# Kernel tuning notes

Hardware: AMD Instinct MI355X
Metric: run time of the kernel (lower is better)

The kernel has to match this reference:

```python
import jax, jax.numpy as jnp
import numpy as np

B, N, D = 8, 4096, 256
K = 8192

def setup_inputs() -> dict:
    key = jax.random.key(0)
    k1, k2 = jax.random.split(key)
    x = jax.random.normal(k1, (B, N, D), dtype=jnp.float32)
    codebook = jax.random.normal(k2, (K, D), dtype=jnp.float32)
    return {"x": x, "codebook": codebook}

def reference(x, codebook):
    """Euclidean VQ forward: cdist + argmin nearest-codebook assignment,
    straight-through quantization, commitment loss, and the scatter-based
    EMA statistics (cluster counts and per-cluster sums)."""
    b, n, d = x.shape
    k = codebook.shape[0]
    flat = x.reshape(-1, d)                                  # [BN, D]
    x2 = jnp.sum(flat * flat, axis=-1, keepdims=True)        # [BN, 1]
    c2 = jnp.sum(codebook * codebook, axis=-1)               # [K]
    dist = x2 + c2[None, :] - 2.0 * (flat @ codebook.T)      # [BN, K]
    embed_ind = jnp.argmin(dist, axis=-1)                    # [BN]
    quantize = codebook[embed_ind].reshape(b, n, d)          # gather
    # commitment loss (codebook detached, as in EMA codebooks)
    commit_loss = jnp.mean((jax.lax.stop_gradient(quantize) - x) ** 2)
    # straight-through estimator
    quantize_st = x + jax.lax.stop_gradient(quantize - x)
    # EMA codebook-update statistics (scatter / segment reductions)
    cluster_size = jax.ops.segment_sum(
        jnp.ones_like(embed_ind, dtype=x.dtype), embed_ind, num_segments=k)  # [K]
    embed_sum = jax.ops.segment_sum(flat, embed_ind, num_segments=k)         # [K, D]
    return quantize_st, embed_ind.reshape(b, n), commit_loss, cluster_size, embed_sum
```

## Files before the change

kernel.cpp:

```cpp
#include <hip/hip_runtime.h>
#include <hip/hip_bf16.h>
#include <math.h>

#define DIM 256
#define KCODES 8192
#define BN_TOTAL 32768

#define OUT_IND 8388608
#define OUT_LOSS 8421376
#define OUT_CS 8421377
#define OUT_ES 8429569
#define OUT_TOTAL 10526721

#define XI8_OFF 0
#define CI8_OFF 4194304
#define PART_OFF OUT_ES

typedef unsigned short u16;
typedef unsigned char u8;
typedef unsigned int u32;
typedef __attribute__((ext_vector_type(4))) int i32x4;
typedef __attribute__((address_space(1))) const void gvoid_t;
typedef __attribute__((address_space(3))) void lvoid_t;

#define QSCALE (127.0f / 6.0f)
#define INV_2S2 (16129.0f / 72.0f)

__global__ __launch_bounds__(256) void vq_prep(const float* __restrict__ x,
                                               const float* __restrict__ cb,
                                               u8* __restrict__ Xi8,
                                               u8* __restrict__ Ci8,
                                               float* __restrict__ c2,
                                               int* __restrict__ c2i) {
  int b = blockIdx.x;
  bool isx = (b < 2048);
  int g = (isx ? b : (b - 2048)) * 256 + threadIdx.x;
  int row = g >> 4;
  int chunk = g & 15;
  const float* src = (isx ? x : cb) + (size_t)row * DIM + chunk * 16;
  float vv[16];
#pragma unroll
  for (int q = 0; q < 4; ++q) {
    float4 v = *(const float4*)(src + q * 4);
    vv[q * 4 + 0] = v.x; vv[q * 4 + 1] = v.y;
    vv[q * 4 + 2] = v.z; vv[q * 4 + 3] = v.w;
  }
  u32 w[4];
  float s = 0.0f;
#pragma unroll
  for (int q = 0; q < 4; ++q) {
    u32 acc = 0;
#pragma unroll
    for (int e = 0; e < 4; ++e) {
      float v = vv[q * 4 + e];
      s += v * v;
      float vs = fminf(fmaxf(v * QSCALE, -127.0f), 127.0f);
      int iv = (int)rintf(vs);
      acc |= ((u32)(u8)(char)iv) << (8 * e);
    }
    w[q] = acc;
  }
  uint4 pk = {w[0], w[1], w[2], w[3]};
  if (isx) {
    *(uint4*)(Xi8 + (size_t)row * DIM + chunk * 16) = pk;
  } else {
    int kbg = chunk >> 2;
    int j = chunk & 3;
    int js = j ^ ((row >> 1) & 3);
    *(uint4*)(Ci8 + (size_t)row * DIM + kbg * 64 + js * 16) = pk;
#pragma unroll
    for (int m = 1; m <= 8; m <<= 1) s += __shfl_xor(s, m, 64);
    if (chunk == 0) {
      c2[row] = s;
      c2i[row] = (int)rintf((s - 256.0f) * INV_2S2);
    }
  }
}

__global__ __launch_bounds__(256, 4)
void vq_mfma(const u8* __restrict__ XB, const u8* __restrict__ CBb,
             const int* __restrict__ c2i, int2* __restrict__ partials) {
  __shared__ __align__(16) u8 As[2][128][64];
  const int t = threadIdx.x;
  const int wid = t >> 6;
  const int lane = t & 63;
  const int lhi = lane >> 4, llo = lane & 15;
  const int sl = lhi ^ ((llo >> 1) & 3);
  const int wm = wid & 1;
  const int wn = wid >> 1;
  const int rt = blockIdx.x & 511;
  const int s = blockIdx.x >> 9;
  const int row0 = rt * 64;
  const int code0base = s * 4096;

  i32x4 b[2][4];
#pragma unroll
  for (int n = 0; n < 2; ++n) {
    const u8* bp = XB + (size_t)(row0 + wn * 32 + n * 16 + llo) * DIM + lhi * 16;
#pragma unroll
    for (int kb = 0; kb < 4; ++kb)
      b[n][kb] = *(const i32x4*)(bp + kb * 64);
  }

  char* AsB = (char*)As;
  const int srow = lane >> 2;
  const int scol = (lane & 3) << 4;

  const int p0 = wid * 2, p1 = wid * 2 + 1;
  const u8* lb0 = CBb + (size_t)(code0base + p0 * 16 + srow) * DIM + scol;
  const u8* lb1 = CBb + (size_t)(code0base + p1 * 16 + srow) * DIM + scol;
  char* dp0 = AsB + (p0 << 10);
  char* dp1 = AsB + (p1 << 10);

  auto STAGE = [&](u32 srcoff, int d) {
    __builtin_amdgcn_global_load_lds((gvoid_t*)(lb0 + srcoff),
                                     (lvoid_t*)(dp0 + (d << 13)), 16, 0, 0);
    __builtin_amdgcn_global_load_lds((gvoid_t*)(lb1 + srcoff),
                                     (lvoid_t*)(dp1 + (d << 13)), 16, 0, 0);
  };

  int v1[2], v2[2];
#pragma unroll
  for (int n = 0; n < 2; ++n) { v1[n] = 0x7FFFFFFF; v2[n] = 0x7FFFFFFF; }

  STAGE(0, 0);
  u32 ctoff = 0;

#pragma unroll 1
  for (int ct = 0; ct < 32; ++ct) {
    const int code0 = code0base + ct * 128;
    i32x4 acc[4][2];
#pragma unroll
    for (int m = 0; m < 4; ++m)
#pragma unroll
      for (int n = 0; n < 2; ++n) acc[m][n] = (i32x4){0, 0, 0, 0};

#pragma unroll
    for (int kb = 0; kb < 4; ++kb) {
      const int cc = ct * 4 + kb;
      __syncthreads();
      if (cc < 127) {
        u32 noff = (kb == 3) ? (ctoff + 32768u) : (ctoff + (u32)(kb + 1) * 64u);
        STAGE(noff, (cc + 1) & 1);
      }
      const char* src = AsB + ((cc & 1) << 13);
      i32x4 a[4];
#pragma unroll
      for (int m = 0; m < 4; ++m)
        a[m] = *(const i32x4*)(src + ((wm * 64 + m * 16 + llo) << 6) + (sl << 4));
#pragma unroll
      for (int m = 0; m < 4; ++m)
#pragma unroll
        for (int n = 0; n < 2; ++n)
          acc[m][n] = __builtin_amdgcn_mfma_i32_16x16x64_i8(a[m], b[n][kb],
                                                            acc[m][n], 0, 0, 0);
      if (kb == 3) {
#pragma unroll
        for (int m = 0; m < 4; ++m) {
          int cbase = code0 + wm * 64 + m * 16 + lhi * 4;
          int4 cv = *(const int4*)(c2i + cbase);
          int cvv[4] = {cv.x, cv.y, cv.z, cv.w};
#pragma unroll
          for (int n = 0; n < 2; ++n) {
#pragma unroll
            for (int r = 0; r < 4; ++r) {
              int diff = cvv[r] - acc[m][n][r];
              int key = (int)(((u32)diff << 13) + (u32)(cbase + r));
              int ov1 = v1[n];
              v1[n] = min(key, ov1);
              v2[n] = min(v2[n], max(key, ov1));
            }
          }
        }
      }
    }
    ctoff += 32768u;
  }
#pragma unroll
  for (int n = 0; n < 2; ++n) {
    int row = row0 + wn * 32 + n * 16 + llo;
    int slot = s * 8 + wm * 4 + lhi;
    partials[(size_t)row * 16 + slot] = make_int2(v1[n], v2[n]);
  }
}

__global__ __launch_bounds__(256)
void vq_pick(const float* __restrict__ x, const float* __restrict__ cb,
             const float* __restrict__ c2g, const int2* __restrict__ partials,
             int* __restrict__ ind, float* __restrict__ out_ind,
             float* __restrict__ out_q, int* __restrict__ cnt,
             float* __restrict__ loss_part) {
  __shared__ float lsm[4];
  int wid = threadIdx.x >> 6, lane = threadIdx.x & 63;
  int row = blockIdx.x * 4 + wid;
  int cv = 0x7FFFFFFF, cv2 = 0x7FFFFFFF;
  if (lane < 16) {
    int2 p = partials[(size_t)row * 16 + lane];
    cv = p.x; cv2 = p.y;
  }
  int cand[4];
#pragma unroll
  for (int rsel = 0; rsel < 4; ++rsel) {
    int bv = cv;
#pragma unroll
    for (int mask = 1; mask < 16; mask <<= 1)
      bv = min(bv, __shfl_xor(bv, mask, 64));
    bv = __shfl(bv, 0, 64);
    cand[rsel] = bv & 8191;
    if (cv == bv) { cv = cv2; cv2 = 0x7FFFFFFF; }
  }
  const float4 xv = *(const float4*)(x + (size_t)row * DIM + lane * 4);
  float4 q0 = *(const float4*)(cb + (size_t)cand[0] * DIM + lane * 4);
  float4 q1 = *(const float4*)(cb + (size_t)cand[1] * DIM + lane * 4);
  float4 q2 = *(const float4*)(cb + (size_t)cand[2] * DIM + lane * 4);
  float4 q3 = *(const float4*)(cb + (size_t)cand[3] * DIM + lane * 4);
  float d0 = xv.x * q0.x + xv.y * q0.y + xv.z * q0.z + xv.w * q0.w;
  float d1 = xv.x * q1.x + xv.y * q1.y + xv.z * q1.z + xv.w * q1.w;
  float d2 = xv.x * q2.x + xv.y * q2.y + xv.z * q2.z + xv.w * q2.w;
  float d3 = xv.x * q3.x + xv.y * q3.y + xv.z * q3.z + xv.w * q3.w;
  float x2 = xv.x * xv.x + xv.y * xv.y + xv.z * xv.z + xv.w * xv.w;
#pragma unroll
  for (int mask = 1; mask < 64; mask <<= 1) {
    d0 += __shfl_xor(d0, mask, 64);
    d1 += __shfl_xor(d1, mask, 64);
    d2 += __shfl_xor(d2, mask, 64);
    d3 += __shfl_xor(d3, mask, 64);
    x2 += __shfl_xor(x2, mask, 64);
  }
  float e0 = fmaf(-2.0f, d0, c2g[cand[0]]);
  float e1 = fmaf(-2.0f, d1, c2g[cand[1]]);
  float e2 = fmaf(-2.0f, d2, c2g[cand[2]]);
  float e3 = fmaf(-2.0f, d3, c2g[cand[3]]);
  float best = e0; int bk = cand[0];
  if (e1 < best || (e1 == best && cand[1] < bk)) { best = e1; bk = cand[1]; }
  if (e2 < best || (e2 == best && cand[2] < bk)) { best = e2; bk = cand[2]; }
  if (e3 < best || (e3 == best && cand[3] < bk)) { best = e3; bk = cand[3]; }
  float4 q = (bk == cand[1]) ? q1 : (bk == cand[2]) ? q2 : (bk == cand[3]) ? q3 : q0;
  *(float4*)(out_q + (size_t)row * DIM + lane * 4) = q;
  if (lane == 0) {
    ind[row] = bk;
    out_ind[row] = (float)bk;
    atomicAdd(cnt + bk, 1);
    lsm[wid] = x2 + best;
  }
  __syncthreads();
  if (threadIdx.x == 0)
    loss_part[blockIdx.x] = lsm[0] + lsm[1] + lsm[2] + lsm[3];
}

__global__ __launch_bounds__(1024)
void vq_scan(const int* __restrict__ cnt, int* __restrict__ offs,
             int* __restrict__ woffs, float* __restrict__ out_cs,
             const float* __restrict__ loss_part, float* __restrict__ out_loss) {
  __shared__ int ssum[1024];
  __shared__ float sls[1024];
  int tid = threadIdx.x;
  int c[8], loc[8];
  int s = 0;
#pragma unroll
  for (int j = 0; j < 8; ++j) {
    c[j] = cnt[tid * 8 + j];
    loc[j] = s;
    s += c[j];
  }
  ssum[tid] = s;
  float ls = 0.0f;
#pragma unroll
  for (int j = 0; j < 8; ++j) ls += loss_part[tid * 8 + j];
  sls[tid] = ls;
  __syncthreads();
  for (int off = 1; off < 1024; off <<= 1) {
    int v = (tid >= off) ? ssum[tid - off] : 0;
    __syncthreads();
    ssum[tid] += v;
    __syncthreads();
  }
  int base = (tid > 0) ? ssum[tid - 1] : 0;
#pragma unroll
  for (int j = 0; j < 8; ++j) {
    int o = base + loc[j];
    offs[tid * 8 + j] = o;
    woffs[tid * 8 + j] = o;
    out_cs[tid * 8 + j] = (float)c[j];
  }
  for (int off = 512; off >= 1; off >>= 1) {
    if (tid < off) sls[tid] += sls[tid + off];
    __syncthreads();
  }
  if (tid == 0) *out_loss = sls[0] * (1.0f / 8388608.0f);
}

__global__ __launch_bounds__(256)
void vq_scatter(const int* __restrict__ ind, int* __restrict__ woffs,
                int* __restrict__ rowlist) {
  int row = blockIdx.x * 256 + threadIdx.x;
  int k = ind[row];
  int pos = atomicAdd(woffs + k, 1);
  rowlist[pos] = row;
}

__global__ __launch_bounds__(256)
void vq_esum(const float* __restrict__ x, const int* __restrict__ offs,
             const int* __restrict__ cnt, const int* __restrict__ rowlist,
             float* __restrict__ out_es) {
  __shared__ float4 sred[3][64];
  int k = blockIdx.x;
  int wid = threadIdx.x >> 6, lane = threadIdx.x & 63;
  int start = offs[k], n = cnt[k];
  const int* rl = rowlist + start;
  int jb = (n * wid) >> 2, je = (n * (wid + 1)) >> 2;
  float4 acc = {0.f, 0.f, 0.f, 0.f};
  int j = jb;
  for (; j + 4 <= je; j += 4) {
    int r0 = rl[j], r1 = rl[j + 1], r2 = rl[j + 2], r3 = rl[j + 3];
    float4 v0 = *(const float4*)(x + (size_t)r0 * DIM + lane * 4);
    float4 v1 = *(const float4*)(x + (size_t)r1 * DIM + lane * 4);
    float4 v2 = *(const float4*)(x + (size_t)r2 * DIM + lane * 4);
    float4 v3 = *(const float4*)(x + (size_t)r3 * DIM + lane * 4);
    acc.x += v0.x + v1.x + v2.x + v3.x;
    acc.y += v0.y + v1.y + v2.y + v3.y;
    acc.z += v0.z + v1.z + v2.z + v3.z;
    acc.w += v0.w + v1.w + v2.w + v3.w;
  }
  for (; j < je; ++j) {
    int r = rl[j];
    float4 v = *(const float4*)(x + (size_t)r * DIM + lane * 4);
    acc.x += v.x; acc.y += v.y; acc.z += v.z; acc.w += v.w;
  }
  if (wid > 0) sred[wid - 1][lane] = acc;
  __syncthreads();
  if (wid == 0) {
    float4 a1 = sred[0][lane], a2 = sred[1][lane], a3 = sred[2][lane];
    acc.x += a1.x + a2.x + a3.x;
    acc.y += a1.y + a2.y + a3.y;
    acc.z += a1.z + a2.z + a3.z;
    acc.w += a1.w + a2.w + a3.w;
    *(float4*)(out_es + (size_t)k * DIM + lane * 4) = acc;
  }
}

extern "C" void kernel_launch(void* const* d_in, const int* in_sizes, int n_in,
                              void* d_out, int out_size, void* d_ws,
                              size_t ws_size, hipStream_t stream) {
  const float* x = (const float*)d_in[0];
  const float* cb = (const float*)d_in[1];
  float* out = (float*)d_out;
  float* out_q = out;
  float* out_ind = out + OUT_IND;
  float* out_loss = out + OUT_LOSS;
  float* out_cs = out + OUT_CS;
  float* out_es = out + OUT_ES;

  u8* Xi8 = (u8*)(out + XI8_OFF);
  u8* Ci8 = (u8*)(out + CI8_OFF);
  int2* partials = (int2*)(out + PART_OFF);

  char* w = (char*)d_ws;
  int* cnt = (int*)w;
  int* offs = (int*)(w + (32 << 10));
  int* woffs = (int*)(w + (64 << 10));
  float* loss_part = (float*)(w + (96 << 10));
  int* ind = (int*)(w + (128 << 10));
  int* rowlist = (int*)(w + (256 << 10));
  float* c2 = (float*)(w + (384 << 10));
  int* c2i = (int*)(w + (416 << 10));

  hipMemsetAsync(cnt, 0, KCODES * sizeof(int), stream);
  vq_prep<<<2560, 256, 0, stream>>>(x, cb, Xi8, Ci8, c2, c2i);
  vq_mfma<<<1024, 256, 0, stream>>>(Xi8, Ci8, c2i, partials);
  vq_pick<<<BN_TOTAL / 4, 256, 0, stream>>>(x, cb, c2, partials, ind, out_ind,
                                            out_q, cnt, loss_part);
  vq_scan<<<1, 1024, 0, stream>>>(cnt, offs, woffs, out_cs, loss_part, out_loss);
  vq_scatter<<<BN_TOTAL / 256, 256, 0, stream>>>(ind, woffs, rowlist);
  vq_esum<<<KCODES, 256, 0, stream>>>(x, offs, cnt, rowlist, out_es);
}
```

Baseline: 178.0 us.

## Give each wave a private codebook ring buffer and drop block-wide barriers in the int8 MFMA kernel

The distance kernel is restructured so each wave owns 64 rows and streams its own 64-code slices of the codebook through a private double-buffered LDS ring, synchronised with explicit vmcnt waits instead of __syncthreads. The per-code c2 values are preloaded into LDS once per block, and the tile grows to 4x4 MFMA accumulators per wave. The grid is halved, so each block covers 2048 codes and writes 4 partial slots per row. The aim is to remove barrier stalls and increase reuse of the X fragments. In exchange it uses more registers (launch bounds lowered to 2 blocks) and loses sharing of codebook tiles across waves, so each wave issues its own global loads.

```diff
diff --git a/kernel.cpp b/kernel.cpp
--- a/kernel.cpp
+++ b/kernel.cpp
@@ -77,109 +77,121 @@
   }
 }
 
-__global__ __launch_bounds__(256, 4)
+__global__ __launch_bounds__(256, 2)
 void vq_mfma(const u8* __restrict__ XB, const u8* __restrict__ CBb,
              const int* __restrict__ c2i, int2* __restrict__ partials) {
-  __shared__ __align__(16) u8 As[2][128][64];
+  __shared__ __align__(16) u8 ring[4][2][4096];
+  __shared__ __align__(16) int c2s[2048];
   const int t = threadIdx.x;
   const int wid = t >> 6;
   const int lane = t & 63;
   const int lhi = lane >> 4, llo = lane & 15;
   const int sl = lhi ^ ((llo >> 1) & 3);
-  const int wm = wid & 1;
-  const int wn = wid >> 1;
-  const int rt = blockIdx.x & 511;
-  const int s = blockIdx.x >> 9;
-  const int row0 = rt * 64;
-  const int code0base = s * 4096;
-
-  i32x4 b[2][4];
-#pragma unroll
-  for (int n = 0; n < 2; ++n) {
-    const u8* bp = XB + (size_t)(row0 + wn * 32 + n * 16 + llo) * DIM + lhi * 16;
-#pragma unroll
-    for (int kb = 0; kb < 4; ++kb)
-      b[n][kb] = *(const i32x4*)(bp + kb * 64);
-  }
-
-  char* AsB = (char*)As;
-  const int srow = lane >> 2;
-  const int scol = (lane & 3) << 4;
-
-  const int p0 = wid * 2, p1 = wid * 2 + 1;
-  const u8* lb0 = CBb + (size_t)(code0base + p0 * 16 + srow) * DIM + scol;
-  const u8* lb1 = CBb + (size_t)(code0base + p1 * 16 + srow) * DIM + scol;
-  char* dp0 = AsB + (p0 << 10);
-  char* dp1 = AsB + (p1 << 10);
-
-  auto STAGE = [&](u32 srcoff, int d) {
-    __builtin_amdgcn_global_load_lds((gvoid_t*)(lb0 + srcoff),
-                                     (lvoid_t*)(dp0 + (d << 13)), 16, 0, 0);
-    __builtin_amdgcn_global_load_lds((gvoid_t*)(lb1 + srcoff),
-                                     (lvoid_t*)(dp1 + (d << 13)), 16, 0, 0);
-  };
-
-  int v1[2], v2[2];
-#pragma unroll
-  for (int n = 0; n < 2; ++n) { v1[n] = 0x7FFFFFFF; v2[n] = 0x7FFFFFFF; }
-
-  STAGE(0, 0);
-  u32 ctoff = 0;
+  const int rg = blockIdx.x & 127;
+  const int s = blockIdx.x >> 7;
+  const int wrow0 = rg * 256 + wid * 64;
+  const int codeS0 = s * 2048;
+
+  i32x4 b[4][4];
+#pragma unroll
+  for (int n = 0; n < 4; ++n) {
+    const u8* bp = XB + (size_t)(wrow0 + n * 16 + llo) * DIM + lhi * 16;
+#pragma unroll
+    for (int kb = 0; kb < 4; ++kb) b[n][kb] = *(const i32x4*)(bp + kb * 64);
+  }
+  {
+    const int* cp = c2i + codeS0 + wid * 512 + lane * 4;
+    char* cd = (char*)c2s + wid * 2048;
+    __builtin_amdgcn_global_load_lds((gvoid_t*)cp, (lvoid_t*)cd, 16, 0, 0);
+    __builtin_amdgcn_global_load_lds((gvoid_t*)(cp + 256), (lvoid_t*)(cd + 1024), 16, 0, 0);
+  }
+  asm volatile("s_waitcnt vmcnt(0)" ::: "memory");
+  __builtin_amdgcn_sched_barrier(0);
+  __syncthreads();
+
+  const u8* sp0 = CBb + (size_t)(codeS0 + (lane >> 2)) * DIM + (lane & 3) * 16;
+  const u8* sp1 = sp0 + (size_t)16 * DIM;
+  const u8* sp2 = sp0 + (size_t)32 * DIM;
+  const u8* sp3 = sp0 + (size_t)48 * DIM;
+  char* rb = (char*)&ring[wid][0][0];
+  const int aoff = llo * 64 + sl * 16;
+
+  int v1[4], v2[4];
+#pragma unroll
+  for (int n = 0; n < 4; ++n) { v1[n] = 0x7FFFFFFF; v2[n] = 0x7FFFFFFF; }
+
+#define STG(BUF, IMM)                                                          \
+  __builtin_amdgcn_global_load_lds((gvoid_t*)(sp0 + (IMM)),                    \
+      (lvoid_t*)(rb + (BUF) * 4096 + 0), 16, 0, 0);                            \
+  __builtin_amdgcn_global_load_lds((gvoid_t*)(sp1 + (IMM)),                    \
+      (lvoid_t*)(rb + (BUF) * 4096 + 1024), 16, 0, 0);                         \
+  __builtin_amdgcn_global_load_lds((gvoid_t*)(sp2 + (IMM)),                    \
+      (lvoid_t*)(rb + (BUF) * 4096 + 2048), 16, 0, 0);                         \
+  __builtin_amdgcn_global_load_lds((gvoid_t*)(sp3 + (IMM)),                    \
+      (lvoid_t*)(rb + (BUF) * 4096 + 3072), 16, 0, 0);
+
+#define VQMM(KB)                                                               \
+  {                                                                            \
+    __builtin_amdgcn_sched_barrier(0);                                         \
+    asm volatile("s_waitcnt vmcnt(4)" ::: "memory");                           \
+    __builtin_amdgcn_sched_barrier(0);                                         \
+    const char* asrc = rb + ((KB) & 1) * 4096;                                 \
+    i32x4 a0 = *(const i32x4*)(asrc + 0 + aoff);                               \
+    i32x4 a1 = *(const i32x4*)(asrc + 1024 + aoff);                            \
+    i32x4 a2 = *(const i32x4*)(asrc + 2048 + aoff);                            \
+    i32x4 a3 = *(const i32x4*)(asrc + 3072 + aoff);                            \
+    _Pragma("unroll")                                                          \
+    for (int n = 0; n < 4; ++n) {                                              \
+      acc[0][n] = __builtin_amdgcn_mfma_i32_16x16x64_i8(a0, b[n][KB], acc[0][n], 0, 0, 0); \
+      acc[1][n] = __builtin_amdgcn_mfma_i32_16x16x64_i8(a1, b[n][KB], acc[1][n], 0, 0, 0); \
+      acc[2][n] = __builtin_amdgcn_mfma_i32_16x16x64_i8(a2, b[n][KB], acc[2][n], 0, 0, 0); \
+      acc[3][n] = __builtin_amdgcn_mfma_i32_16x16x64_i8(a3, b[n][KB], acc[3][n], 0, 0, 0); \
+    }                                                                          \
+  }
+
+  STG(0, 0);
 
 #pragma unroll 1
   for (int ct = 0; ct < 32; ++ct) {
-    const int code0 = code0base + ct * 128;
-    i32x4 acc[4][2];
+    i32x4 acc[4][4];
 #pragma unroll
     for (int m = 0; m < 4; ++m)
 #pragma unroll
-      for (int n = 0; n < 2; ++n) acc[m][n] = (i32x4){0, 0, 0, 0};
-
-#pragma unroll
-    for (int kb = 0; kb < 4; ++kb) {
-      const int cc = ct * 4 + kb;
-      __syncthreads();
-      if (cc < 127) {
-        u32 noff = (kb == 3) ? (ctoff + 32768u) : (ctoff + (u32)(kb + 1) * 64u);
-        STAGE(noff, (cc + 1) & 1);
-      }
-      const char* src = AsB + ((cc & 1) << 13);
-      i32x4 a[4];
-#pragma unroll
-      for (int m = 0; m < 4; ++m)
-        a[m] = *(const i32x4*)(src + ((wm * 64 + m * 16 + llo) << 6) + (sl << 4));
-#pragma unroll
-      for (int m = 0; m < 4; ++m)
-#pragma unroll
-        for (int n = 0; n < 2; ++n)
-          acc[m][n] = __builtin_amdgcn_mfma_i32_16x16x64_i8(a[m], b[n][kb],
-                                                            acc[m][n], 0, 0, 0);
-      if (kb == 3) {
-#pragma unroll
-        for (int m = 0; m < 4; ++m) {
-          int cbase = code0 + wm * 64 + m * 16 + lhi * 4;
-          int4 cv = *(const int4*)(c2i + cbase);
-          int cvv[4] = {cv.x, cv.y, cv.z, cv.w};
-#pragma unroll
-          for (int n = 0; n < 2; ++n) {
-#pragma unroll
-            for (int r = 0; r < 4; ++r) {
-              int diff = cvv[r] - acc[m][n][r];
-              int key = (int)(((u32)diff << 13) + (u32)(cbase + r));
-              int ov1 = v1[n];
-              v1[n] = min(key, ov1);
-              v2[n] = min(v2[n], max(key, ov1));
-            }
-          }
+      for (int n = 0; n < 4; ++n) acc[m][n] = (i32x4){0, 0, 0, 0};
+
+    STG(1, 64);   VQMM(0)
+    STG(0, 128);  VQMM(1)
+    STG(1, 192);  VQMM(2)
+    sp0 += 16384; sp1 += 16384; sp2 += 16384; sp3 += 16384;
+    STG(0, 0);    VQMM(3)
+
+    const int ctb = ct * 256;
+#pragma unroll
+    for (int m = 0; m < 4; ++m) {
+      int4 cv = *(const int4*)((const char*)c2s + ctb + m * 64 + lhi * 16);
+      int cbase = codeS0 + ct * 64 + m * 16 + lhi * 4;
+      int cvv[4] = {cv.x, cv.y, cv.z, cv.w};
+#pragma unroll
+      for (int n = 0; n < 4; ++n) {
+#pragma unroll
+        for (int r = 0; r < 4; ++r) {
+          int diff = cvv[r] - acc[m][n][r];
+          int key = (int)(((u32)diff << 13) + (u32)(cbase + r));
+          int ov1 = v1[n];
+          v1[n] = min(key, ov1);
+          v2[n] = min(v2[n], max(key, ov1));
         }
       }
     }
-    ctoff += 32768u;
-  }
-#pragma unroll
-  for (int n = 0; n < 2; ++n) {
-    int row = row0 + wn * 32 + n * 16 + llo;
-    int slot = s * 8 + wm * 4 + lhi;
+  }
+#undef STG
+#undef VQMM
+  asm volatile("s_waitcnt vmcnt(0)" ::: "memory");
+
+#pragma unroll
+  for (int n = 0; n < 4; ++n) {
+    int row = wrow0 + n * 16 + llo;
+    int slot = s * 4 + lhi;
     partials[(size_t)row * 16 + slot] = make_int2(v1[n], v2[n]);
   }
 }
@@ -367,7 +379,7 @@
 
   hipMemsetAsync(cnt, 0, KCODES * sizeof(int), stream);
   vq_prep<<<2560, 256, 0, stream>>>(x, cb, Xi8, Ci8, c2, c2i);
-  vq_mfma<<<1024, 256, 0, stream>>>(Xi8, Ci8, c2i, partials);
+  vq_mfma<<<512, 256, 0, stream>>>(Xi8, Ci8, c2i, partials);
   vq_pick<<<BN_TOTAL / 4, 256, 0, stream>>>(x, cb, c2, partials, ind, out_ind,
                                             out_q, cnt, loss_part);
   vq_scan<<<1, 1024, 0, stream>>>(cnt, offs, woffs, out_cs, loss_part, out_loss);
```

Measured after the change: 158.8 us. 10.8% less time.
